# Kernel optimization log

Hardware: AMD Instinct MI355X
Metric: run time of the kernel (lower is better)

Reference implementation:

```python
import jax, jax.numpy as jnp
import numpy as np

N, F_IN, F_OUT = 8192, 512, 256
NEG_BIG = -9e15


def setup_inputs() -> dict:
    key = jax.random.key(0)
    k1, k2, k3, k4, k5 = jax.random.split(key, 5)
    h = jax.random.normal(k1, (N, F_IN), dtype=jnp.float32)
    adj = jax.random.randint(k2, (N, N), 0, 2, dtype=jnp.int32)
    W = jax.random.normal(k3, (F_IN, F_OUT), dtype=jnp.float32) / np.sqrt(F_IN)
    bW = jnp.zeros((F_OUT,), dtype=jnp.float32)
    a1 = jax.random.normal(k4, (F_OUT,), dtype=jnp.float32) / np.sqrt(2 * F_OUT)
    a2 = jax.random.normal(k5, (F_OUT,), dtype=jnp.float32) / np.sqrt(2 * F_OUT)
    ba = jnp.zeros((), dtype=jnp.float32)
    return {"h": h, "adj": adj, "W": W, "bW": bW, "a1": a1, "a2": a2, "ba": ba}


def reference(h, adj, W, bW, a1, a2, ba):
    # Wh: [N, F_OUT]
    Wh = h @ W + bW
    # a([Wh_i ; Wh_j]) + b == (Wh_i . a1) + (Wh_j . a2) + b  (rank-1 decomposition,
    # avoids the O(N^2 * 2F) repeat/cat tensor the torch code materializes)
    f1 = Wh @ a1  # [N]
    f2 = Wh @ a2  # [N]
    e = jax.nn.leaky_relu(f1[:, None] + f2[None, :] + ba, negative_slope=0.2)
    e = jnp.where(adj > 0, e, NEG_BIG)
    attention = jax.nn.softmax(e, axis=1)  # dropout = identity (eval mode)
    return attention @ Wh
```

## Files before the change

### kernel.cpp

```cpp
#include <hip/hip_runtime.h>

typedef __bf16 bf16;
typedef __attribute__((ext_vector_type(4))) float f32x4;
typedef __attribute__((ext_vector_type(8))) __bf16 bf16x8;
typedef __attribute__((ext_vector_type(4))) __bf16 bf16x4;
typedef __attribute__((ext_vector_type(4))) int i32x4;

#define NN 8192
#define FI 512
#define FO 256
#define NSPLIT 8
#define JCHUNK (NN / NSPLIT)
#define KSTEPS (JCHUNK / 32)

__global__ __launch_bounds__(256) void kw_split(const float* __restrict__ W,
                                                bf16* __restrict__ wth,
                                                bf16* __restrict__ wtl) {
  const int idx = blockIdx.x * 256 + threadIdx.x;
  const int k = idx >> 8, n = idx & 255;
  float x = W[idx];
  bf16 hi = (bf16)x;
  wth[(size_t)n * FI + k] = hi;
  wtl[(size_t)n * FI + k] = (bf16)(x - (float)hi);
}

__global__ __launch_bounds__(256) void k1_gemm(
    const float* __restrict__ h, const bf16* __restrict__ wth,
    const bf16* __restrict__ wtl, const float* __restrict__ bW,
    const float* __restrict__ a1, const float* __restrict__ a2,
    bf16* __restrict__ whb, float* __restrict__ f1, float* __restrict__ f2) {
  __shared__ bf16 Ah[32 * 40];
  __shared__ bf16 Al[32 * 40];
  const int t = threadIdx.x;
  const int lane = t & 63, w = t >> 6;
  const int m16 = lane & 15, q = lane >> 4;
  const int bi = blockIdx.x, bj = blockIdx.y;
  const int i0 = bi * 32;
  const int n0 = bj * 128 + w * 32;
  const int srow = t >> 3, skoff = (t & 7) * 4;

  const f32x4 z4 = {0.f, 0.f, 0.f, 0.f};
  f32x4 acc[2][2];
#pragma unroll
  for (int mt = 0; mt < 2; ++mt)
#pragma unroll
    for (int nt = 0; nt < 2; ++nt) acc[mt][nt] = z4;

  const float* hrow = h + (size_t)(i0 + srow) * FI + skoff;

  for (int kt = 0; kt < FI / 32; ++kt) {
    f32x4 hv = *(const f32x4*)(hrow + kt * 32);
    bf16x8 bh[2], bl[2];
#pragma unroll
    for (int nt = 0; nt < 2; ++nt) {
      const size_t woff = (size_t)(n0 + nt * 16 + m16) * FI + kt * 32 + q * 8;
      bh[nt] = *(const bf16x8*)(wth + woff);
      bl[nt] = *(const bf16x8*)(wtl + woff);
    }
    bf16x4 hh, hl;
#pragma unroll
    for (int x = 0; x < 4; ++x) {
      float v = hv[x];
      bf16 hi = (bf16)v;
      hh[x] = hi;
      hl[x] = (bf16)(v - (float)hi);
    }
    __syncthreads();
    *(bf16x4*)&Ah[srow * 40 + skoff] = hh;
    *(bf16x4*)&Al[srow * 40 + skoff] = hl;
    __syncthreads();
#pragma unroll
    for (int mt = 0; mt < 2; ++mt) {
      bf16x8 ah = *(const bf16x8*)&Ah[(mt * 16 + m16) * 40 + q * 8];
      bf16x8 al = *(const bf16x8*)&Al[(mt * 16 + m16) * 40 + q * 8];
#pragma unroll
      for (int nt = 0; nt < 2; ++nt) {
        acc[mt][nt] = __builtin_amdgcn_mfma_f32_16x16x32_bf16(ah, bh[nt], acc[mt][nt], 0, 0, 0);
        acc[mt][nt] = __builtin_amdgcn_mfma_f32_16x16x32_bf16(al, bh[nt], acc[mt][nt], 0, 0, 0);
        acc[mt][nt] = __builtin_amdgcn_mfma_f32_16x16x32_bf16(ah, bl[nt], acc[mt][nt], 0, 0, 0);
      }
    }
  }
  float f1p[2][4] = {}, f2p[2][4] = {};
#pragma unroll
  for (int nt = 0; nt < 2; ++nt) {
    const int n = n0 + nt * 16 + m16;
    const float bw = bW[n], av1 = a1[n], av2 = a2[n];
#pragma unroll
    for (int mt = 0; mt < 2; ++mt) {
#pragma unroll
      for (int reg = 0; reg < 4; ++reg) {
        float wh = acc[mt][nt][reg] + bw;
        const int il = mt * 16 + q * 4 + reg;
        whb[(size_t)bi * (FO * 32) + n * 32 + il] = (bf16)wh;
        f1p[mt][reg] += wh * av1;
        f2p[mt][reg] += wh * av2;
      }
    }
  }
#pragma unroll
  for (int m = 1; m < 16; m <<= 1) {
#pragma unroll
    for (int mt = 0; mt < 2; ++mt)
#pragma unroll
      for (int reg = 0; reg < 4; ++reg) {
        f1p[mt][reg] += __shfl_xor(f1p[mt][reg], m);
        f2p[mt][reg] += __shfl_xor(f2p[mt][reg], m);
      }
  }
  if (m16 == 0) {
#pragma unroll
    for (int mt = 0; mt < 2; ++mt)
#pragma unroll
      for (int reg = 0; reg < 4; ++reg) {
        const int i = i0 + mt * 16 + q * 4 + reg;
        atomicAdd(&f1[i], f1p[mt][reg]);
        atomicAdd(&f2[i], f2p[mt][reg]);
      }
  }
}

__global__ __launch_bounds__(256) void k3_max(const float* __restrict__ f2,
                                              float* __restrict__ Mstar) {
  __shared__ float red[4];
  const int t = threadIdx.x;
  float m = -1e30f;
  for (int i = t; i < NN; i += 256) m = fmaxf(m, f2[i]);
#pragma unroll
  for (int d = 1; d < 64; d <<= 1) m = fmaxf(m, __shfl_xor(m, d));
  if ((t & 63) == 0) red[t >> 6] = m;
  __syncthreads();
  if (t == 0) *Mstar = fmaxf(fmaxf(red[0], red[1]), fmaxf(red[2], red[3]));
}

__global__ __launch_bounds__(256) void k4_attn(
    const int* __restrict__ adj, const bf16* __restrict__ whb,
    const float* __restrict__ f1, const float* __restrict__ f2,
    const float* __restrict__ Mstar, const float* __restrict__ ba_p,
    float* __restrict__ acc_part, float* __restrict__ l_part) {
  __shared__ bf16 Pl[64 * 40];
  const int t = threadIdx.x;
  const int lane = t & 63, w = t >> 6;
  const int m16 = lane & 15, q = lane >> 4;
  const int rb = blockIdx.x, s = blockIdx.y;
  const int i0 = rb * 64;
  const int rloc = t >> 2;
  const int jj = (t & 3) * 8;

  const float ba = *ba_p;
  const float Ms = *Mstar;
  const float ci = f1[i0 + rloc] + ba;
  float sh = ci + Ms;
  sh = fmaxf(sh, 0.2f * sh);

  const f32x4 z4 = {0.f, 0.f, 0.f, 0.f};
  f32x4 acc[4][4];
#pragma unroll
  for (int mt = 0; mt < 4; ++mt)
#pragma unroll
    for (int cc = 0; cc < 4; ++cc) acc[mt][cc] = z4;
  float lreg = 0.f;

  const int* arow = adj + (size_t)(i0 + rloc) * NN;
  const int sbase = s * JCHUNK;

  i32x4 a4a = *(const i32x4*)(arow + sbase + jj);
  i32x4 a4b = *(const i32x4*)(arow + sbase + jj + 4);
  f32x4 s4a = *(const f32x4*)(f2 + sbase + jj);
  f32x4 s4b = *(const f32x4*)(f2 + sbase + jj + 4);
  bf16x8 bfr[4];
  {
    const size_t bbase = (size_t)(sbase >> 5) * (FO * 32) + q * 8;
#pragma unroll
    for (int cc = 0; cc < 4; ++cc)
      bfr[cc] = *(const bf16x8*)(whb + bbase + (size_t)((w * 4 + cc) * 16 + m16) * 32);
  }

  for (int kt = 0; kt < KSTEPS; ++kt) {
    float pv[8];
#pragma unroll
    for (int x = 0; x < 4; ++x) {
      float arg = ci + s4a[x];
      float e = fmaxf(arg, 0.2f * arg);
      pv[x] = (a4a[x] > 0) ? __expf(e - sh) : 0.f;
    }
#pragma unroll
    for (int x = 0; x < 4; ++x) {
      float arg = ci + s4b[x];
      float e = fmaxf(arg, 0.2f * arg);
      pv[4 + x] = (a4b[x] > 0) ? __expf(e - sh) : 0.f;
    }
#pragma unroll
    for (int x = 0; x < 8; ++x) lreg += pv[x];
    bf16x8 pb;
#pragma unroll
    for (int x = 0; x < 8; ++x) pb[x] = (bf16)pv[x];

    const int ktn = (kt + 1 < KSTEPS) ? kt + 1 : kt;
    const int j0n = sbase + ktn * 32;
    i32x4 a4a_n = *(const i32x4*)(arow + j0n + jj);
    i32x4 a4b_n = *(const i32x4*)(arow + j0n + jj + 4);
    f32x4 s4a_n = *(const f32x4*)(f2 + j0n + jj);
    f32x4 s4b_n = *(const f32x4*)(f2 + j0n + jj + 4);
    bf16x8 bfn[4];
    const size_t bbn = (size_t)(j0n >> 5) * (FO * 32) + q * 8;
#pragma unroll
    for (int cc = 0; cc < 4; ++cc)
      bfn[cc] = *(const bf16x8*)(whb + bbn + (size_t)((w * 4 + cc) * 16 + m16) * 32);

    __syncthreads();
    *(bf16x8*)&Pl[rloc * 40 + jj] = pb;
    __syncthreads();

#pragma unroll
    for (int mt = 0; mt < 4; ++mt) {
      bf16x8 af = *(const bf16x8*)&Pl[(mt * 16 + m16) * 40 + q * 8];
#pragma unroll
      for (int cc = 0; cc < 4; ++cc)
        acc[mt][cc] = __builtin_amdgcn_mfma_f32_16x16x32_bf16(af, bfr[cc], acc[mt][cc], 0, 0, 0);
    }
    a4a = a4a_n; a4b = a4b_n; s4a = s4a_n; s4b = s4b_n;
#pragma unroll
    for (int cc = 0; cc < 4; ++cc) bfr[cc] = bfn[cc];
  }
  lreg += __shfl_xor(lreg, 1);
  lreg += __shfl_xor(lreg, 2);
  if ((t & 3) == 0) l_part[(size_t)s * NN + i0 + rloc] = lreg;
  float* ap = acc_part + (size_t)s * ((size_t)NN * FO);
#pragma unroll
  for (int mt = 0; mt < 4; ++mt) {
#pragma unroll
    for (int cc = 0; cc < 4; ++cc) {
      const int n = (w * 4 + cc) * 16 + m16;
#pragma unroll
      for (int reg = 0; reg < 4; ++reg) {
        const int r = i0 + mt * 16 + q * 4 + reg;
        ap[(size_t)r * FO + n] = acc[mt][cc][reg];
      }
    }
  }
}

__global__ __launch_bounds__(256) void k5_reduce(
    const float* __restrict__ accp, const float* __restrict__ lp,
    float* __restrict__ out) {
  const int idx = blockIdx.x * 256 + threadIdx.x;
  const int i = idx >> 6, n4 = (idx & 63) * 4;
  f32x4 sum = {0.f, 0.f, 0.f, 0.f};
  float l = 0.f;
#pragma unroll
  for (int s = 0; s < NSPLIT; ++s) {
    sum += *(const f32x4*)&accp[(size_t)s * ((size_t)NN * FO) + (size_t)i * FO + n4];
    l += lp[s * NN + i];
  }
  const float rl = 1.0f / l;
  f32x4 o = sum * rl;
  *(f32x4*)&out[(size_t)i * FO + n4] = o;
}

extern "C" void kernel_launch(void* const* d_in, const int* in_sizes, int n_in,
                              void* d_out, int out_size, void* d_ws, size_t ws_size,
                              hipStream_t stream) {
  const float* h   = (const float*)d_in[0];
  const int*   adj = (const int*)d_in[1];
  const float* W   = (const float*)d_in[2];
  const float* bW  = (const float*)d_in[3];
  const float* a1  = (const float*)d_in[4];
  const float* a2  = (const float*)d_in[5];
  const float* ba  = (const float*)d_in[6];
  float* out = (float*)d_out;

  char* ws = (char*)d_ws;
  bf16* whb   = (bf16*)ws;
  float* f1   = (float*)(ws + 4u * 1024 * 1024);
  float* f2   = (float*)(ws + 4u * 1024 * 1024 + 32 * 1024);
  float* Mst  = (float*)(ws + 4u * 1024 * 1024 + 64 * 1024);
  float* accp = (float*)(ws + 4u * 1024 * 1024 + 64 * 1024 + 256);
  float* lp   = accp + (size_t)NSPLIT * NN * FO;
  bf16* wth   = (bf16*)((char*)lp + (size_t)NSPLIT * NN * 4);
  bf16* wtl   = wth + (size_t)FO * FI;

  hipMemsetAsync(f1, 0, 64 * 1024, stream);

  kw_split<<<FI * FO / 256, 256, 0, stream>>>(W, wth, wtl);
  k1_gemm<<<dim3(NN / 32, 2), 256, 0, stream>>>(h, wth, wtl, bW, a1, a2, whb, f1, f2);
  k3_max<<<1, 256, 0, stream>>>(f2, Mst);
  k4_attn<<<dim3(NN / 64, NSPLIT), 256, 0, stream>>>(adj, whb, f1, f2, Mst, ba, accp, lp);
  k5_reduce<<<(NN * FO / 4) / 256, 256, 0, stream>>>(accp, lp, out);
}
```

Baseline: 490.2 us.

## Compute attention probabilities directly in MFMA A-fragment layout, drop LDS staging

Each wave now owns 16 rows and all 256 output columns, and computes the attention probabilities straight into its MFMA A-operand registers. This removes the shared-memory round trip and the two barriers per k-step. In exchange, every wave loads the full Wh tile for the k-step (16 B-fragments per iteration instead of 4), which raises global/L2 traffic on Wh fourfold. The B fragments are also no longer prefetched a step ahead. A launch-bounds occupancy hint of 3 blocks is added.

```diff
diff --git a/kernel.cpp b/kernel.cpp
--- a/kernel.cpp
+++ b/kernel.cpp
@@ -133,50 +133,48 @@
   if (t == 0) *Mstar = fmaxf(fmaxf(red[0], red[1]), fmaxf(red[2], red[3]));
 }
 
-__global__ __launch_bounds__(256) void k4_attn(
+__global__ __launch_bounds__(256, 3) void k4_attn(
     const int* __restrict__ adj, const bf16* __restrict__ whb,
     const float* __restrict__ f1, const float* __restrict__ f2,
     const float* __restrict__ Mstar, const float* __restrict__ ba_p,
     float* __restrict__ acc_part, float* __restrict__ l_part) {
-  __shared__ bf16 Pl[64 * 40];
   const int t = threadIdx.x;
   const int lane = t & 63, w = t >> 6;
   const int m16 = lane & 15, q = lane >> 4;
   const int rb = blockIdx.x, s = blockIdx.y;
   const int i0 = rb * 64;
-  const int rloc = t >> 2;
-  const int jj = (t & 3) * 8;
+  const int row = i0 + w * 16 + m16;
+  const int jq = q * 8;
 
   const float ba = *ba_p;
   const float Ms = *Mstar;
-  const float ci = f1[i0 + rloc] + ba;
+  const float ci = f1[row] + ba;
   float sh = ci + Ms;
   sh = fmaxf(sh, 0.2f * sh);
 
   const f32x4 z4 = {0.f, 0.f, 0.f, 0.f};
-  f32x4 acc[4][4];
-#pragma unroll
-  for (int mt = 0; mt < 4; ++mt)
-#pragma unroll
-    for (int cc = 0; cc < 4; ++cc) acc[mt][cc] = z4;
+  f32x4 acc[16];
+#pragma unroll
+  for (int cc = 0; cc < 16; ++cc) acc[cc] = z4;
   float lreg = 0.f;
 
-  const int* arow = adj + (size_t)(i0 + rloc) * NN;
+  const int* arow = adj + (size_t)row * NN;
   const int sbase = s * JCHUNK;
 
-  i32x4 a4a = *(const i32x4*)(arow + sbase + jj);
-  i32x4 a4b = *(const i32x4*)(arow + sbase + jj + 4);
-  f32x4 s4a = *(const f32x4*)(f2 + sbase + jj);
-  f32x4 s4b = *(const f32x4*)(f2 + sbase + jj + 4);
-  bf16x8 bfr[4];
-  {
-    const size_t bbase = (size_t)(sbase >> 5) * (FO * 32) + q * 8;
-#pragma unroll
-    for (int cc = 0; cc < 4; ++cc)
-      bfr[cc] = *(const bf16x8*)(whb + bbase + (size_t)((w * 4 + cc) * 16 + m16) * 32);
-  }
+  i32x4 a4a = *(const i32x4*)(arow + sbase + jq);
+  i32x4 a4b = *(const i32x4*)(arow + sbase + jq + 4);
+  f32x4 s4a = *(const f32x4*)(f2 + sbase + jq);
+  f32x4 s4b = *(const f32x4*)(f2 + sbase + jq + 4);
 
   for (int kt = 0; kt < KSTEPS; ++kt) {
+    const int j0 = sbase + kt * 32;
+    const int ktn = (kt + 1 < KSTEPS) ? kt + 1 : kt;
+    const int j0n = sbase + ktn * 32;
+    i32x4 a4a_n = *(const i32x4*)(arow + j0n + jq);
+    i32x4 a4b_n = *(const i32x4*)(arow + j0n + jq + 4);
+    f32x4 s4a_n = *(const f32x4*)(f2 + j0n + jq);
+    f32x4 s4b_n = *(const f32x4*)(f2 + j0n + jq + 4);
+
     float pv[8];
 #pragma unroll
     for (int x = 0; x < 4; ++x) {
@@ -192,51 +190,29 @@
     }
 #pragma unroll
     for (int x = 0; x < 8; ++x) lreg += pv[x];
-    bf16x8 pb;
-#pragma unroll
-    for (int x = 0; x < 8; ++x) pb[x] = (bf16)pv[x];
-
-    const int ktn = (kt + 1 < KSTEPS) ? kt + 1 : kt;
-    const int j0n = sbase + ktn * 32;
-    i32x4 a4a_n = *(const i32x4*)(arow + j0n + jj);
-    i32x4 a4b_n = *(const i32x4*)(arow + j0n + jj + 4);
-    f32x4 s4a_n = *(const f32x4*)(f2 + j0n + jj);
-    f32x4 s4b_n = *(const f32x4*)(f2 + j0n + jj + 4);
-    bf16x8 bfn[4];
-    const size_t bbn = (size_t)(j0n >> 5) * (FO * 32) + q * 8;
-#pragma unroll
-    for (int cc = 0; cc < 4; ++cc)
-      bfn[cc] = *(const bf16x8*)(whb + bbn + (size_t)((w * 4 + cc) * 16 + m16) * 32);
-
-    __syncthreads();
-    *(bf16x8*)&Pl[rloc * 40 + jj] = pb;
-    __syncthreads();
-
-#pragma unroll
-    for (int mt = 0; mt < 4; ++mt) {
-      bf16x8 af = *(const bf16x8*)&Pl[(mt * 16 + m16) * 40 + q * 8];
-#pragma unroll
-      for (int cc = 0; cc < 4; ++cc)
-        acc[mt][cc] = __builtin_amdgcn_mfma_f32_16x16x32_bf16(af, bfr[cc], acc[mt][cc], 0, 0, 0);
+    bf16x8 af;
+#pragma unroll
+    for (int x = 0; x < 8; ++x) af[x] = (bf16)pv[x];
+
+    const size_t bbase = (size_t)(j0 >> 5) * (FO * 32) + q * 8;
+#pragma unroll
+    for (int cc = 0; cc < 16; ++cc) {
+      bf16x8 bfr = *(const bf16x8*)(whb + bbase + (size_t)(cc * 16 + m16) * 32);
+      acc[cc] = __builtin_amdgcn_mfma_f32_16x16x32_bf16(af, bfr, acc[cc], 0, 0, 0);
     }
     a4a = a4a_n; a4b = a4b_n; s4a = s4a_n; s4b = s4b_n;
-#pragma unroll
-    for (int cc = 0; cc < 4; ++cc) bfr[cc] = bfn[cc];
-  }
-  lreg += __shfl_xor(lreg, 1);
-  lreg += __shfl_xor(lreg, 2);
-  if ((t & 3) == 0) l_part[(size_t)s * NN + i0 + rloc] = lreg;
+  }
+  lreg += __shfl_xor(lreg, 16);
+  lreg += __shfl_xor(lreg, 32);
+  if (q == 0) l_part[(size_t)s * NN + row] = lreg;
   float* ap = acc_part + (size_t)s * ((size_t)NN * FO);
 #pragma unroll
-  for (int mt = 0; mt < 4; ++mt) {
-#pragma unroll
-    for (int cc = 0; cc < 4; ++cc) {
-      const int n = (w * 4 + cc) * 16 + m16;
-#pragma unroll
-      for (int reg = 0; reg < 4; ++reg) {
-        const int r = i0 + mt * 16 + q * 4 + reg;
-        ap[(size_t)r * FO + n] = acc[mt][cc][reg];
-      }
+  for (int cc = 0; cc < 16; ++cc) {
+    const int n = cc * 16 + m16;
+#pragma unroll
+    for (int reg = 0; reg < 4; ++reg) {
+      const int r = i0 + w * 16 + q * 4 + reg;
+      ap[(size_t)r * FO + n] = acc[cc][reg];
     }
   }
 }
```

Measured after the change: 657.6 us. 1.34x slower.

## Compute attention probabilities directly in MFMA A-fragment layout, dropping LDS staging

Applied to the files above, without the earlier changes.

Each wave now computes the exp/mask probabilities for all 64 rows itself, laid out exactly as the MFMA A operand wants them. This removes the shared-memory staging buffer and both per-step __syncthreads. In exchange every wave repeats the exp and adjacency work (four times the elementwise compute and adjacency loads per block) and uses more registers. The Wh B-fragment prefetch is also dropped, and launch bounds now request two blocks per CU.

```diff
diff --git a/kernel.cpp b/kernel.cpp
--- a/kernel.cpp
+++ b/kernel.cpp
@@ -133,109 +133,121 @@
   if (t == 0) *Mstar = fmaxf(fmaxf(red[0], red[1]), fmaxf(red[2], red[3]));
 }
 
-__global__ __launch_bounds__(256) void k4_attn(
+__global__ __launch_bounds__(256, 2) void k4_attn(
     const int* __restrict__ adj, const bf16* __restrict__ whb,
     const float* __restrict__ f1, const float* __restrict__ f2,
     const float* __restrict__ Mstar, const float* __restrict__ ba_p,
     float* __restrict__ acc_part, float* __restrict__ l_part) {
-  __shared__ bf16 Pl[64 * 40];
   const int t = threadIdx.x;
   const int lane = t & 63, w = t >> 6;
   const int m16 = lane & 15, q = lane >> 4;
   const int rb = blockIdx.x, s = blockIdx.y;
   const int i0 = rb * 64;
-  const int rloc = t >> 2;
-  const int jj = (t & 3) * 8;
+  const int jq = q * 8;
 
   const float ba = *ba_p;
   const float Ms = *Mstar;
-  const float ci = f1[i0 + rloc] + ba;
-  float sh = ci + Ms;
-  sh = fmaxf(sh, 0.2f * sh);
+  float ci[4], sh[4];
+  const int* arow[4];
+#pragma unroll
+  for (int rt = 0; rt < 4; ++rt) {
+    const int r = i0 + rt * 16 + m16;
+    ci[rt] = f1[r] + ba;
+    float v = ci[rt] + Ms;
+    sh[rt] = fmaxf(v, 0.2f * v);
+    arow[rt] = adj + (size_t)r * NN;
+  }
 
   const f32x4 z4 = {0.f, 0.f, 0.f, 0.f};
   f32x4 acc[4][4];
 #pragma unroll
-  for (int mt = 0; mt < 4; ++mt)
-#pragma unroll
-    for (int cc = 0; cc < 4; ++cc) acc[mt][cc] = z4;
-  float lreg = 0.f;
-
-  const int* arow = adj + (size_t)(i0 + rloc) * NN;
+  for (int rt = 0; rt < 4; ++rt)
+#pragma unroll
+    for (int cc = 0; cc < 4; ++cc) acc[rt][cc] = z4;
+  float lreg[4] = {0.f, 0.f, 0.f, 0.f};
+
   const int sbase = s * JCHUNK;
 
-  i32x4 a4a = *(const i32x4*)(arow + sbase + jj);
-  i32x4 a4b = *(const i32x4*)(arow + sbase + jj + 4);
-  f32x4 s4a = *(const f32x4*)(f2 + sbase + jj);
-  f32x4 s4b = *(const f32x4*)(f2 + sbase + jj + 4);
-  bf16x8 bfr[4];
-  {
-    const size_t bbase = (size_t)(sbase >> 5) * (FO * 32) + q * 8;
+  i32x4 a0[4], a1r[4];
+  f32x4 fa0, fa1;
+#pragma unroll
+  for (int rt = 0; rt < 4; ++rt) {
+    a0[rt] = *(const i32x4*)(arow[rt] + sbase + jq);
+    a1r[rt] = *(const i32x4*)(arow[rt] + sbase + jq + 4);
+  }
+  fa0 = *(const f32x4*)(f2 + sbase + jq);
+  fa1 = *(const f32x4*)(f2 + sbase + jq + 4);
+
+  for (int kt = 0; kt < KSTEPS; ++kt) {
+    const int j0 = sbase + kt * 32;
+
+    bf16x8 bfr[4];
+    const size_t bbase = (size_t)(j0 >> 5) * (FO * 32) + jq;
 #pragma unroll
     for (int cc = 0; cc < 4; ++cc)
       bfr[cc] = *(const bf16x8*)(whb + bbase + (size_t)((w * 4 + cc) * 16 + m16) * 32);
-  }
-
-  for (int kt = 0; kt < KSTEPS; ++kt) {
-    float pv[8];
-#pragma unroll
-    for (int x = 0; x < 4; ++x) {
-      float arg = ci + s4a[x];
-      float e = fmaxf(arg, 0.2f * arg);
-      pv[x] = (a4a[x] > 0) ? __expf(e - sh) : 0.f;
-    }
-#pragma unroll
-    for (int x = 0; x < 4; ++x) {
-      float arg = ci + s4b[x];
-      float e = fmaxf(arg, 0.2f * arg);
-      pv[4 + x] = (a4b[x] > 0) ? __expf(e - sh) : 0.f;
-    }
-#pragma unroll
-    for (int x = 0; x < 8; ++x) lreg += pv[x];
-    bf16x8 pb;
-#pragma unroll
-    for (int x = 0; x < 8; ++x) pb[x] = (bf16)pv[x];
 
     const int ktn = (kt + 1 < KSTEPS) ? kt + 1 : kt;
     const int j0n = sbase + ktn * 32;
-    i32x4 a4a_n = *(const i32x4*)(arow + j0n + jj);
-    i32x4 a4b_n = *(const i32x4*)(arow + j0n + jj + 4);
-    f32x4 s4a_n = *(const f32x4*)(f2 + j0n + jj);
-    f32x4 s4b_n = *(const f32x4*)(f2 + j0n + jj + 4);
-    bf16x8 bfn[4];
-    const size_t bbn = (size_t)(j0n >> 5) * (FO * 32) + q * 8;
-#pragma unroll
-    for (int cc = 0; cc < 4; ++cc)
-      bfn[cc] = *(const bf16x8*)(whb + bbn + (size_t)((w * 4 + cc) * 16 + m16) * 32);
-
-    __syncthreads();
-    *(bf16x8*)&Pl[rloc * 40 + jj] = pb;
-    __syncthreads();
-
-#pragma unroll
-    for (int mt = 0; mt < 4; ++mt) {
-      bf16x8 af = *(const bf16x8*)&Pl[(mt * 16 + m16) * 40 + q * 8];
+    i32x4 a0n[4], a1n[4];
+#pragma unroll
+    for (int rt = 0; rt < 4; ++rt) {
+      a0n[rt] = *(const i32x4*)(arow[rt] + j0n + jq);
+      a1n[rt] = *(const i32x4*)(arow[rt] + j0n + jq + 4);
+    }
+    f32x4 fa0n = *(const f32x4*)(f2 + j0n + jq);
+    f32x4 fa1n = *(const f32x4*)(f2 + j0n + jq + 4);
+
+    bf16x8 af[4];
+#pragma unroll
+    for (int rt = 0; rt < 4; ++rt) {
+      float pv[8];
+#pragma unroll
+      for (int x = 0; x < 4; ++x) {
+        float arg = ci[rt] + fa0[x];
+        float e = fmaxf(arg, 0.2f * arg);
+        pv[x] = (a0[rt][x] > 0) ? __expf(e - sh[rt]) : 0.f;
+      }
+#pragma unroll
+      for (int x = 0; x < 4; ++x) {
+        float arg = ci[rt] + fa1[x];
+        float e = fmaxf(arg, 0.2f * arg);
+        pv[4 + x] = (a1r[rt][x] > 0) ? __expf(e - sh[rt]) : 0.f;
+      }
+#pragma unroll
+      for (int x = 0; x < 8; ++x) lreg[rt] += pv[x];
+#pragma unroll
+      for (int x = 0; x < 8; ++x) af[rt][x] = (bf16)pv[x];
+    }
+
+#pragma unroll
+    for (int rt = 0; rt < 4; ++rt)
 #pragma unroll
       for (int cc = 0; cc < 4; ++cc)
-        acc[mt][cc] = __builtin_amdgcn_mfma_f32_16x16x32_bf16(af, bfr[cc], acc[mt][cc], 0, 0, 0);
-    }
-    a4a = a4a_n; a4b = a4b_n; s4a = s4a_n; s4b = s4b_n;
-#pragma unroll
-    for (int cc = 0; cc < 4; ++cc) bfr[cc] = bfn[cc];
-  }
-  lreg += __shfl_xor(lreg, 1);
-  lreg += __shfl_xor(lreg, 2);
-  if ((t & 3) == 0) l_part[(size_t)s * NN + i0 + rloc] = lreg;
+        acc[rt][cc] = __builtin_amdgcn_mfma_f32_16x16x32_bf16(af[rt], bfr[cc], acc[rt][cc], 0, 0, 0);
+
+#pragma unroll
+    for (int rt = 0; rt < 4; ++rt) { a0[rt] = a0n[rt]; a1r[rt] = a1n[rt]; }
+    fa0 = fa0n; fa1 = fa1n;
+  }
+
+#pragma unroll
+  for (int rt = 0; rt < 4; ++rt) {
+    float lr = lreg[rt];
+    lr += __shfl_xor(lr, 16);
+    lr += __shfl_xor(lr, 32);
+    if (q == 0) l_part[(size_t)s * NN + i0 + rt * 16 + m16] = lr;
+  }
   float* ap = acc_part + (size_t)s * ((size_t)NN * FO);
 #pragma unroll
-  for (int mt = 0; mt < 4; ++mt) {
+  for (int rt = 0; rt < 4; ++rt) {
 #pragma unroll
     for (int cc = 0; cc < 4; ++cc) {
       const int n = (w * 4 + cc) * 16 + m16;
 #pragma unroll
       for (int reg = 0; reg < 4; ++reg) {
-        const int r = i0 + mt * 16 + q * 4 + reg;
-        ap[(size_t)r * FO + n] = acc[mt][cc][reg];
+        const int r = i0 + rt * 16 + q * 4 + reg;
+        ap[(size_t)r * FO + n] = acc[rt][cc][reg];
       }
     }
   }
```

After: 517.0 us. 1.05x slower.
